# Kernel optimization log

Measured on AMD Instinct MI355X. Metric: run time of the kernel, lower is better.

The kernel has to match this reference:

```python
import jax, jax.numpy as jnp
import numpy as np


def _chamfer(xyz1, xyz2):
    # xyz1: [B, N, 3], xyz2: [B, M, 3]
    sq1 = jnp.sum(xyz1 * xyz1, axis=-1)            # [B, N]
    sq2 = jnp.sum(xyz2 * xyz2, axis=-1)            # [B, M]
    inner = jnp.einsum('bnd,bmd->bnm', xyz1, xyz2) # [B, N, M]
    d = sq1[:, :, None] + sq2[:, None, :] - 2.0 * inner
    d = jnp.maximum(d, 0.0)  # guard tiny negatives from cancellation
    dist1 = jnp.min(d, axis=2)  # [B, N] nearest in xyz2 for each point of xyz1
    dist2 = jnp.min(d, axis=1)  # [B, M]
    return jnp.mean(dist1) + jnp.mean(dist2)


def setup_inputs() -> dict:
    key = jax.random.key(0)
    k1, k2 = jax.random.split(key)
    B, N, M = 16, 4096, 4096
    xyz1 = jax.random.normal(k1, (B, N, 3), dtype=jnp.float32)
    xyz2 = jax.random.normal(k2, (B, M, 3), dtype=jnp.float32)
    return {"xyz1": xyz1, "xyz2": xyz2}


def reference(xyz1, xyz2):
    return _chamfer(xyz1, xyz2)
```

## Files before the change

kernel.cpp:

```cpp
#include <hip/hip_runtime.h>


#define BATCH 16
#define NPTS  4096
#define NQ_TOTAL (BATCH * NPTS)

typedef __attribute__((ext_vector_type(8)))  short bf16x8;
typedef __attribute__((ext_vector_type(16))) float f32x16;
typedef __attribute__((ext_vector_type(4)))  unsigned int u32x4;

union FragCast { bf16x8 v; u32x4 u; };

__device__ __forceinline__ unsigned short bf16_rne(float v) {
    unsigned u = __float_as_uint(v);
    u += 0x7FFFu + ((u >> 16) & 1u);
    return (unsigned short)(u >> 16);
}
__device__ __forceinline__ float bf16f(unsigned short h) {
    return __uint_as_float(((unsigned)h) << 16);
}

__global__ __launch_bounds__(256, 2) void chamfer_fused_kernel(
    const float* __restrict__ xyz1, const float* __restrict__ xyz2,
    float* __restrict__ partials)
{
    const int orig = (int)blockIdx.x;
    const int wfid = (orig & 7) * 64 + (orig >> 3);
    const int og = wfid & 15;
    const int b  = (wfid >> 4) & 15;
    const int d  = wfid >> 8;

    const int tid = (int)threadIdx.x;
    const int wid = tid >> 6;
    const int l   = tid & 63;
    const int c   = l & 31;
    const int g   = l >> 5;
    const int strip0 = og * 8 + wid;
    const int strip1 = og * 8 + wid + 4;

    const float* qpts = d ? xyz2 : xyz1;
    const float* tpts = d ? xyz1 : xyz2;

    const unsigned short one = 0x3F80;
    bf16x8 af0, af1;
    #pragma unroll
    for (int s = 0; s < 2; ++s) {
        const int strip = s ? strip1 : strip0;
        const int qi = b * NPTS + strip * 32 + c;
        const float qx = qpts[qi * 3 + 0];
        const float qy = qpts[qi * 3 + 1];
        const float qz = qpts[qi * 3 + 2];
        const float mx = -2.0f * qx, my = -2.0f * qy, mz = -2.0f * qz;
        const float Q  = fmaf(qx, qx, fmaf(qy, qy, qz * qz));
        const unsigned short xh = bf16_rne(mx), xl = bf16_rne(mx - bf16f(xh));
        const unsigned short yh = bf16_rne(my), yl = bf16_rne(my - bf16f(yh));
        const unsigned short zh = bf16_rne(mz), zl = bf16_rne(mz - bf16f(zh));
        const unsigned short Qh = bf16_rne(Q),  Ql = bf16_rne(Q - bf16f(Qh));
        bf16x8 af;
        if (g == 0) {
            af[0] = (short)xh; af[1] = (short)xh; af[2] = (short)xl; af[3] = (short)yh;
            af[4] = (short)yh; af[5] = (short)yl; af[6] = (short)zh; af[7] = (short)zh;
        } else {
            af[0] = (short)zl; af[1] = (short)one; af[2] = (short)one; af[3] = (short)Qh;
            af[4] = (short)Ql; af[5] = 0;          af[6] = 0;          af[7] = 0;
        }
        if (s) af1 = af; else af0 = af;
    }

    f32x16 vzero;
    #pragma unroll
    for (int i = 0; i < 16; ++i) vzero[i] = 0.0f;

    f32x16 rm0, rm1;
    #pragma unroll
    for (int i = 0; i < 16; ++i) { rm0[i] = 1e30f; rm1[i] = 1e30f; }

    __shared__ u32x4 lds[64 * 64];

    for (int cc = 0; cc < 2; ++cc) {
        __syncthreads();

        const float* tb = tpts + ((size_t)b * NPTS + (size_t)cc * 2048) * 3;
        #pragma unroll
        for (int k = 0; k < 8; ++k) {
            const int pi = k * 256 + tid;
            const float x = tb[pi * 3 + 0];
            const float y = tb[pi * 3 + 1];
            const float z = tb[pi * 3 + 2];
            const float S = fmaf(x, x, fmaf(y, y, z * z));
            const unsigned short Xh = bf16_rne(x), Xl = bf16_rne(x - bf16f(Xh));
            const unsigned short Yh = bf16_rne(y), Yl = bf16_rne(y - bf16f(Yh));
            const unsigned short Zh = bf16_rne(z), Zl = bf16_rne(z - bf16f(Zh));
            const unsigned short Sh = bf16_rne(S), Sl = bf16_rne(S - bf16f(Sh));
            FragCast f0, f1;
            f0.v[0] = (short)Xh; f0.v[1] = (short)Xl; f0.v[2] = (short)Xh; f0.v[3] = (short)Yh;
            f0.v[4] = (short)Yl; f0.v[5] = (short)Yh; f0.v[6] = (short)Zh; f0.v[7] = (short)Zl;
            f1.v[0] = (short)Zh; f1.v[1] = (short)Sh; f1.v[2] = (short)Sl; f1.v[3] = (short)one;
            f1.v[4] = (short)one; f1.v[5] = 0;        f1.v[6] = 0;         f1.v[7] = 0;
            const int t  = pi >> 5;
            const int c2 = pi & 31;
            lds[t * 64 + c2]      = f0.u;
            lds[t * 64 + 32 + c2] = f1.u;
        }
        __syncthreads();

        #pragma unroll 2
        for (int t = 0; t < 64; t += 2) {
            FragCast ta, tb2;
            ta.u  = lds[(t + 0) * 64 + l];
            tb2.u = lds[(t + 1) * 64 + l];
            f32x16 a0 = __builtin_amdgcn_mfma_f32_32x32x16_bf16(af0, ta.v,  vzero, 0, 0, 0);
            f32x16 a1 = __builtin_amdgcn_mfma_f32_32x32x16_bf16(af0, tb2.v, vzero, 0, 0, 0);
            f32x16 b0 = __builtin_amdgcn_mfma_f32_32x32x16_bf16(af1, ta.v,  vzero, 0, 0, 0);
            f32x16 b1 = __builtin_amdgcn_mfma_f32_32x32x16_bf16(af1, tb2.v, vzero, 0, 0, 0);
            #pragma unroll
            for (int i = 0; i < 16; ++i) {
                rm0[i] = fminf(fminf(rm0[i], a0[i]), a1[i]);
                rm1[i] = fminf(fminf(rm1[i], b0[i]), b1[i]);
            }
        }
    }

    #pragma unroll
    for (int m = 1; m <= 16; m <<= 1) {
        #pragma unroll
        for (int i = 0; i < 16; ++i) {
            rm0[i] = fminf(rm0[i], __shfl_xor(rm0[i], m, 64));
            rm1[i] = fminf(rm1[i], __shfl_xor(rm1[i], m, 64));
        }
    }

    float s0 = 0.0f, s1 = 0.0f;
    #pragma unroll
    for (int i = 0; i < 16; ++i) {
        s0 += fmaxf(rm0[i], 0.0f);
        s1 += fmaxf(rm1[i], 0.0f);
    }
    s0 += __shfl_xor(s0, 32, 64);
    s1 += __shfl_xor(s1, 32, 64);
    const float s = s0 + s1;

    __shared__ float wsum[4];
    if (l == 0) wsum[wid] = s;
    __syncthreads();
    if (tid == 0)
        partials[orig] = wsum[0] + wsum[1] + wsum[2] + wsum[3];
}

__global__ __launch_bounds__(256) void final_kernel(
    const float* __restrict__ partials, float* __restrict__ out)
{
    const int t = (int)threadIdx.x;
    float v = partials[t] + partials[t + 256];

    #pragma unroll
    for (int off = 32; off >= 1; off >>= 1)
        v += __shfl_down(v, off, 64);

    __shared__ float wsum[4];
    const int lane = t & 63;
    const int wid  = t >> 6;
    if (lane == 0) wsum[wid] = v;
    __syncthreads();
    if (t == 0)
        out[0] = (wsum[0] + wsum[1] + wsum[2] + wsum[3]) * (1.0f / (float)NQ_TOTAL);
}

extern "C" void kernel_launch(void* const* d_in, const int* in_sizes, int n_in,
                              void* d_out, int out_size, void* d_ws, size_t ws_size,
                              hipStream_t stream) {
    const float* xyz1 = (const float*)d_in[0];
    const float* xyz2 = (const float*)d_in[1];
    float* out = (float*)d_out;
    float* partials = (float*)d_ws;

    chamfer_fused_kernel<<<512, 256, 0, stream>>>(xyz1, xyz2, partials);
    final_kernel<<<1, 256, 0, stream>>>(partials, out);
}
```

Measured before the change: 27.08 us.

## Give each wave four query strips over half the targets, merge mins in LDS

```diff
diff --git a/kernel.cpp b/kernel.cpp
--- a/kernel.cpp
+++ b/kernel.cpp
@@ -18,6 +18,30 @@
 }
 __device__ __forceinline__ float bf16f(unsigned short h) {
     return __uint_as_float(((unsigned)h) << 16);
+}
+
+__device__ __forceinline__ bf16x8 build_af(const float* __restrict__ qpts,
+                                           int b, int strip, int c, int g) {
+    const int qi = b * NPTS + strip * 32 + c;
+    const float qx = qpts[qi * 3 + 0];
+    const float qy = qpts[qi * 3 + 1];
+    const float qz = qpts[qi * 3 + 2];
+    const float mx = -2.0f * qx, my = -2.0f * qy, mz = -2.0f * qz;
+    const float Q  = fmaf(qx, qx, fmaf(qy, qy, qz * qz));
+    const unsigned short xh = bf16_rne(mx), xl = bf16_rne(mx - bf16f(xh));
+    const unsigned short yh = bf16_rne(my), yl = bf16_rne(my - bf16f(yh));
+    const unsigned short zh = bf16_rne(mz), zl = bf16_rne(mz - bf16f(zh));
+    const unsigned short Qh = bf16_rne(Q),  Ql = bf16_rne(Q - bf16f(Qh));
+    const unsigned short one = 0x3F80;
+    bf16x8 af;
+    if (g == 0) {
+        af[0] = (short)xh; af[1] = (short)xh; af[2] = (short)xl; af[3] = (short)yh;
+        af[4] = (short)yh; af[5] = (short)yl; af[6] = (short)zh; af[7] = (short)zh;
+    } else {
+        af[0] = (short)zl; af[1] = (short)one; af[2] = (short)one; af[3] = (short)Qh;
+        af[4] = (short)Ql; af[5] = 0;          af[6] = 0;          af[7] = 0;
+    }
+    return af;
 }
 
 __global__ __launch_bounds__(256, 2) void chamfer_fused_kernel(
@@ -26,7 +50,7 @@
 {
     const int orig = (int)blockIdx.x;
     const int wfid = (orig & 7) * 64 + (orig >> 3);
-    const int og = wfid & 15;
+    const int sg = wfid & 15;
     const int b  = (wfid >> 4) & 15;
     const int d  = wfid >> 8;
 
@@ -35,58 +59,43 @@
     const int l   = tid & 63;
     const int c   = l & 31;
     const int g   = l >> 5;
-    const int strip0 = og * 8 + wid;
-    const int strip1 = og * 8 + wid + 4;
+    const int qw  = wid & 1;
+    const int h   = wid >> 1;
 
     const float* qpts = d ? xyz2 : xyz1;
     const float* tpts = d ? xyz1 : xyz2;
 
+    const bf16x8 af0 = build_af(qpts, b, sg * 8 + qw * 4 + 0, c, g);
+    const bf16x8 af1 = build_af(qpts, b, sg * 8 + qw * 4 + 1, c, g);
+    const bf16x8 af2 = build_af(qpts, b, sg * 8 + qw * 4 + 2, c, g);
+    const bf16x8 af3 = build_af(qpts, b, sg * 8 + qw * 4 + 3, c, g);
+
+    f32x16 vzero;
+    #pragma unroll
+    for (int i = 0; i < 16; ++i) vzero[i] = 0.0f;
+
+    f32x16 rm0, rm1, rm2, rm3;
+    #pragma unroll
+    for (int i = 0; i < 16; ++i) { rm0[i] = 1e30f; rm1[i] = 1e30f; rm2[i] = 1e30f; rm3[i] = 1e30f; }
+
+    __shared__ u32x4 lds[2048];
+    __shared__ float lmin[4][128];
+
     const unsigned short one = 0x3F80;
-    bf16x8 af0, af1;
-    #pragma unroll
-    for (int s = 0; s < 2; ++s) {
-        const int strip = s ? strip1 : strip0;
-        const int qi = b * NPTS + strip * 32 + c;
-        const float qx = qpts[qi * 3 + 0];
-        const float qy = qpts[qi * 3 + 1];
-        const float qz = qpts[qi * 3 + 2];
-        const float mx = -2.0f * qx, my = -2.0f * qy, mz = -2.0f * qz;
-        const float Q  = fmaf(qx, qx, fmaf(qy, qy, qz * qz));
-        const unsigned short xh = bf16_rne(mx), xl = bf16_rne(mx - bf16f(xh));
-        const unsigned short yh = bf16_rne(my), yl = bf16_rne(my - bf16f(yh));
-        const unsigned short zh = bf16_rne(mz), zl = bf16_rne(mz - bf16f(zh));
-        const unsigned short Qh = bf16_rne(Q),  Ql = bf16_rne(Q - bf16f(Qh));
-        bf16x8 af;
-        if (g == 0) {
-            af[0] = (short)xh; af[1] = (short)xh; af[2] = (short)xl; af[3] = (short)yh;
-            af[4] = (short)yh; af[5] = (short)yl; af[6] = (short)zh; af[7] = (short)zh;
-        } else {
-            af[0] = (short)zl; af[1] = (short)one; af[2] = (short)one; af[3] = (short)Qh;
-            af[4] = (short)Ql; af[5] = 0;          af[6] = 0;          af[7] = 0;
-        }
-        if (s) af1 = af; else af0 = af;
-    }
-
-    f32x16 vzero;
-    #pragma unroll
-    for (int i = 0; i < 16; ++i) vzero[i] = 0.0f;
-
-    f32x16 rm0, rm1;
-    #pragma unroll
-    for (int i = 0; i < 16; ++i) { rm0[i] = 1e30f; rm1[i] = 1e30f; }
-
-    __shared__ u32x4 lds[64 * 64];
-
-    for (int cc = 0; cc < 2; ++cc) {
+    const float* tptr = tpts + (size_t)b * NPTS * 3;
+
+    for (int p = 0; p < 4; ++p) {
         __syncthreads();
 
-        const float* tb = tpts + ((size_t)b * NPTS + (size_t)cc * 2048) * 3;
         #pragma unroll
-        for (int k = 0; k < 8; ++k) {
-            const int pi = k * 256 + tid;
-            const float x = tb[pi * 3 + 0];
-            const float y = tb[pi * 3 + 1];
-            const float z = tb[pi * 3 + 2];
+        for (int k = 0; k < 4; ++k) {
+            const int pi  = k * 256 + tid;
+            const int h2  = pi >> 9;
+            const int idx = pi & 511;
+            const int gp  = h2 * 2048 + p * 512 + idx;
+            const float x = tptr[gp * 3 + 0];
+            const float y = tptr[gp * 3 + 1];
+            const float z = tptr[gp * 3 + 2];
             const float S = fmaf(x, x, fmaf(y, y, z * z));
             const unsigned short Xh = bf16_rne(x), Xl = bf16_rne(x - bf16f(Xh));
             const unsigned short Yh = bf16_rne(y), Yl = bf16_rne(y - bf16f(Yh));
@@ -97,26 +106,36 @@
             f0.v[4] = (short)Yl; f0.v[5] = (short)Yh; f0.v[6] = (short)Zh; f0.v[7] = (short)Zl;
             f1.v[0] = (short)Zh; f1.v[1] = (short)Sh; f1.v[2] = (short)Sl; f1.v[3] = (short)one;
             f1.v[4] = (short)one; f1.v[5] = 0;        f1.v[6] = 0;         f1.v[7] = 0;
-            const int t  = pi >> 5;
-            const int c2 = pi & 31;
-            lds[t * 64 + c2]      = f0.u;
-            lds[t * 64 + 32 + c2] = f1.u;
+            const int t  = idx >> 5;
+            const int c2 = idx & 31;
+            lds[h2 * 1024 + t * 64 + c2]      = f0.u;
+            lds[h2 * 1024 + t * 64 + 32 + c2] = f1.u;
         }
         __syncthreads();
 
+        const int lbase = h * 1024 + l;
         #pragma unroll 2
-        for (int t = 0; t < 64; t += 2) {
-            FragCast ta, tb2;
-            ta.u  = lds[(t + 0) * 64 + l];
-            tb2.u = lds[(t + 1) * 64 + l];
-            f32x16 a0 = __builtin_amdgcn_mfma_f32_32x32x16_bf16(af0, ta.v,  vzero, 0, 0, 0);
-            f32x16 a1 = __builtin_amdgcn_mfma_f32_32x32x16_bf16(af0, tb2.v, vzero, 0, 0, 0);
-            f32x16 b0 = __builtin_amdgcn_mfma_f32_32x32x16_bf16(af1, ta.v,  vzero, 0, 0, 0);
-            f32x16 b1 = __builtin_amdgcn_mfma_f32_32x32x16_bf16(af1, tb2.v, vzero, 0, 0, 0);
+        for (int t = 0; t < 16; t += 2) {
+            FragCast ta, tb;
+            ta.u = lds[lbase + (t + 0) * 64];
+            tb.u = lds[lbase + (t + 1) * 64];
+            f32x16 o0a = __builtin_amdgcn_mfma_f32_32x32x16_bf16(af0, ta.v, vzero, 0, 0, 0);
+            f32x16 o0b = __builtin_amdgcn_mfma_f32_32x32x16_bf16(af0, tb.v, vzero, 0, 0, 0);
+            f32x16 o1a = __builtin_amdgcn_mfma_f32_32x32x16_bf16(af1, ta.v, vzero, 0, 0, 0);
+            f32x16 o1b = __builtin_amdgcn_mfma_f32_32x32x16_bf16(af1, tb.v, vzero, 0, 0, 0);
             #pragma unroll
             for (int i = 0; i < 16; ++i) {
-                rm0[i] = fminf(fminf(rm0[i], a0[i]), a1[i]);
-                rm1[i] = fminf(fminf(rm1[i], b0[i]), b1[i]);
+                rm0[i] = fminf(rm0[i], fminf(o0a[i], o0b[i]));
+                rm1[i] = fminf(rm1[i], fminf(o1a[i], o1b[i]));
+            }
+            f32x16 o2a = __builtin_amdgcn_mfma_f32_32x32x16_bf16(af2, ta.v, vzero, 0, 0, 0);
+            f32x16 o2b = __builtin_amdgcn_mfma_f32_32x32x16_bf16(af2, tb.v, vzero, 0, 0, 0);
+            f32x16 o3a = __builtin_amdgcn_mfma_f32_32x32x16_bf16(af3, ta.v, vzero, 0, 0, 0);
+            f32x16 o3b = __builtin_amdgcn_mfma_f32_32x32x16_bf16(af3, tb.v, vzero, 0, 0, 0);
+            #pragma unroll
+            for (int i = 0; i < 16; ++i) {
+                rm2[i] = fminf(rm2[i], fminf(o2a[i], o2b[i]));
+                rm3[i] = fminf(rm3[i], fminf(o3a[i], o3b[i]));
             }
         }
     }
@@ -127,21 +146,33 @@
         for (int i = 0; i < 16; ++i) {
             rm0[i] = fminf(rm0[i], __shfl_xor(rm0[i], m, 64));
             rm1[i] = fminf(rm1[i], __shfl_xor(rm1[i], m, 64));
-        }
-    }
-
-    float s0 = 0.0f, s1 = 0.0f;
-    #pragma unroll
-    for (int i = 0; i < 16; ++i) {
-        s0 += fmaxf(rm0[i], 0.0f);
-        s1 += fmaxf(rm1[i], 0.0f);
-    }
-    s0 += __shfl_xor(s0, 32, 64);
-    s1 += __shfl_xor(s1, 32, 64);
-    const float s = s0 + s1;
+            rm2[i] = fminf(rm2[i], __shfl_xor(rm2[i], m, 64));
+            rm3[i] = fminf(rm3[i], __shfl_xor(rm3[i], m, 64));
+        }
+    }
+
+    if (c == 0) {
+        #pragma unroll
+        for (int i = 0; i < 16; ++i) {
+            const int row = (i & 3) + 8 * (i >> 2) + 4 * g;
+            lmin[wid][0 * 32 + row] = rm0[i];
+            lmin[wid][1 * 32 + row] = rm1[i];
+            lmin[wid][2 * 32 + row] = rm2[i];
+            lmin[wid][3 * 32 + row] = rm3[i];
+        }
+    }
+    __syncthreads();
+
+    const int qw2  = tid >> 7;
+    const int idx2 = tid & 127;
+    float v = fmaxf(fminf(lmin[qw2][idx2], lmin[qw2 + 2][idx2]), 0.0f);
+
+    #pragma unroll
+    for (int off = 32; off >= 1; off >>= 1)
+        v += __shfl_down(v, off, 64);
 
     __shared__ float wsum[4];
-    if (l == 0) wsum[wid] = s;
+    if (l == 0) wsum[wid] = v;
     __syncthreads();
     if (tid == 0)
         partials[orig] = wsum[0] + wsum[1] + wsum[2] + wsum[3];
```

After: 49.01 us. 81.0% more time.

## Double-buffer target tiles in LDS, prefetching next chunk during MFMA loop

Applied to the files above, without the earlier changes.

```diff
diff --git a/kernel.cpp b/kernel.cpp
--- a/kernel.cpp
+++ b/kernel.cpp
@@ -18,6 +18,23 @@
 }
 __device__ __forceinline__ float bf16f(unsigned short h) {
     return __uint_as_float(((unsigned)h) << 16);
+}
+
+__device__ __forceinline__ void pack_pt(float x, float y, float z,
+                                        u32x4* f0u, u32x4* f1u) {
+    const float S = fmaf(x, x, fmaf(y, y, z * z));
+    const unsigned short Xh = bf16_rne(x), Xl = bf16_rne(x - bf16f(Xh));
+    const unsigned short Yh = bf16_rne(y), Yl = bf16_rne(y - bf16f(Yh));
+    const unsigned short Zh = bf16_rne(z), Zl = bf16_rne(z - bf16f(Zh));
+    const unsigned short Sh = bf16_rne(S), Sl = bf16_rne(S - bf16f(Sh));
+    const unsigned short one = 0x3F80;
+    FragCast f0, f1;
+    f0.v[0] = (short)Xh; f0.v[1] = (short)Xl; f0.v[2] = (short)Xh; f0.v[3] = (short)Yh;
+    f0.v[4] = (short)Yl; f0.v[5] = (short)Yh; f0.v[6] = (short)Zh; f0.v[7] = (short)Zl;
+    f1.v[0] = (short)Zh; f1.v[1] = (short)Sh; f1.v[2] = (short)Sl; f1.v[3] = (short)one;
+    f1.v[4] = (short)one; f1.v[5] = 0;        f1.v[6] = 0;         f1.v[7] = 0;
+    *f0u = f0.u;
+    *f1u = f1.u;
 }
 
 __global__ __launch_bounds__(256, 2) void chamfer_fused_kernel(
@@ -33,7 +50,7 @@
     const int tid = (int)threadIdx.x;
     const int wid = tid >> 6;
     const int l   = tid & 63;
-    const int c   = l & 31;
+    const int lc  = l & 31;
     const int g   = l >> 5;
     const int strip0 = og * 8 + wid;
     const int strip1 = og * 8 + wid + 4;
@@ -46,7 +63,7 @@
     #pragma unroll
     for (int s = 0; s < 2; ++s) {
         const int strip = s ? strip1 : strip0;
-        const int qi = b * NPTS + strip * 32 + c;
+        const int qi = b * NPTS + strip * 32 + lc;
         const float qx = qpts[qi * 3 + 0];
         const float qy = qpts[qi * 3 + 1];
         const float qz = qpts[qi * 3 + 2];
@@ -75,50 +92,69 @@
     #pragma unroll
     for (int i = 0; i < 16; ++i) { rm0[i] = 1e30f; rm1[i] = 1e30f; }
 
-    __shared__ u32x4 lds[64 * 64];
-
-    for (int cc = 0; cc < 2; ++cc) {
-        __syncthreads();
-
-        const float* tb = tpts + ((size_t)b * NPTS + (size_t)cc * 2048) * 3;
-        #pragma unroll
-        for (int k = 0; k < 8; ++k) {
-            const int pi = k * 256 + tid;
-            const float x = tb[pi * 3 + 0];
-            const float y = tb[pi * 3 + 1];
-            const float z = tb[pi * 3 + 2];
-            const float S = fmaf(x, x, fmaf(y, y, z * z));
-            const unsigned short Xh = bf16_rne(x), Xl = bf16_rne(x - bf16f(Xh));
-            const unsigned short Yh = bf16_rne(y), Yl = bf16_rne(y - bf16f(Yh));
-            const unsigned short Zh = bf16_rne(z), Zl = bf16_rne(z - bf16f(Zh));
-            const unsigned short Sh = bf16_rne(S), Sl = bf16_rne(S - bf16f(Sh));
-            FragCast f0, f1;
-            f0.v[0] = (short)Xh; f0.v[1] = (short)Xl; f0.v[2] = (short)Xh; f0.v[3] = (short)Yh;
-            f0.v[4] = (short)Yl; f0.v[5] = (short)Yh; f0.v[6] = (short)Zh; f0.v[7] = (short)Zl;
-            f1.v[0] = (short)Zh; f1.v[1] = (short)Sh; f1.v[2] = (short)Sl; f1.v[3] = (short)one;
-            f1.v[4] = (short)one; f1.v[5] = 0;        f1.v[6] = 0;         f1.v[7] = 0;
-            const int t  = pi >> 5;
-            const int c2 = pi & 31;
-            lds[t * 64 + c2]      = f0.u;
-            lds[t * 64 + 32 + c2] = f1.u;
-        }
-        __syncthreads();
+    __shared__ u32x4 lds[2][32 * 64];
+
+    const float* tptr = tpts + (size_t)b * NPTS * 3;
+
+    #pragma unroll
+    for (int k = 0; k < 4; ++k) {
+        const int pi = k * 256 + tid;
+        const float x = tptr[pi * 3 + 0];
+        const float y = tptr[pi * 3 + 1];
+        const float z = tptr[pi * 3 + 2];
+        u32x4 f0u, f1u;
+        pack_pt(x, y, z, &f0u, &f1u);
+        const int t  = pi >> 5;
+        const int c2 = pi & 31;
+        lds[0][t * 64 + c2]      = f0u;
+        lds[0][t * 64 + 32 + c2] = f1u;
+    }
+    __syncthreads();
+
+    #pragma unroll
+    for (int cc = 0; cc < 4; ++cc) {
+        const int cur = cc & 1;
+
+        float px[4], py[4], pz[4];
+        if (cc < 3) {
+            #pragma unroll
+            for (int k = 0; k < 4; ++k) {
+                const int gp = (cc + 1) * 1024 + k * 256 + tid;
+                px[k] = tptr[gp * 3 + 0];
+                py[k] = tptr[gp * 3 + 1];
+                pz[k] = tptr[gp * 3 + 2];
+            }
+        }
 
         #pragma unroll 2
-        for (int t = 0; t < 64; t += 2) {
+        for (int t = 0; t < 32; t += 2) {
             FragCast ta, tb2;
-            ta.u  = lds[(t + 0) * 64 + l];
-            tb2.u = lds[(t + 1) * 64 + l];
+            ta.u  = lds[cur][(t + 0) * 64 + l];
+            tb2.u = lds[cur][(t + 1) * 64 + l];
             f32x16 a0 = __builtin_amdgcn_mfma_f32_32x32x16_bf16(af0, ta.v,  vzero, 0, 0, 0);
             f32x16 a1 = __builtin_amdgcn_mfma_f32_32x32x16_bf16(af0, tb2.v, vzero, 0, 0, 0);
             f32x16 b0 = __builtin_amdgcn_mfma_f32_32x32x16_bf16(af1, ta.v,  vzero, 0, 0, 0);
             f32x16 b1 = __builtin_amdgcn_mfma_f32_32x32x16_bf16(af1, tb2.v, vzero, 0, 0, 0);
             #pragma unroll
             for (int i = 0; i < 16; ++i) {
-                rm0[i] = fminf(fminf(rm0[i], a0[i]), a1[i]);
-                rm1[i] = fminf(fminf(rm1[i], b0[i]), b1[i]);
+                rm0[i] = fminf(rm0[i], fminf(a0[i], a1[i]));
+                rm1[i] = fminf(rm1[i], fminf(b0[i], b1[i]));
             }
         }
+
+        if (cc < 3) {
+            #pragma unroll
+            for (int k = 0; k < 4; ++k) {
+                const int pi = k * 256 + tid;
+                u32x4 f0u, f1u;
+                pack_pt(px[k], py[k], pz[k], &f0u, &f1u);
+                const int t  = pi >> 5;
+                const int c2 = pi & 31;
+                lds[cur ^ 1][t * 64 + c2]      = f0u;
+                lds[cur ^ 1][t * 64 + 32 + c2] = f1u;
+            }
+        }
+        __syncthreads();
     }
 
     #pragma unroll
```

Result: slower. 42.56 us (+57.2%).

## Split target loop across two wave halves with 512-thread blocks and LDS min merge

Applied to the files above, without the earlier changes.

```diff
diff --git a/kernel.cpp b/kernel.cpp
--- a/kernel.cpp
+++ b/kernel.cpp
@@ -20,7 +20,7 @@
     return __uint_as_float(((unsigned)h) << 16);
 }
 
-__global__ __launch_bounds__(256, 2) void chamfer_fused_kernel(
+__global__ __launch_bounds__(512, 4) void chamfer_fused_kernel(
     const float* __restrict__ xyz1, const float* __restrict__ xyz2,
     float* __restrict__ partials)
 {
@@ -33,10 +33,12 @@
     const int tid = (int)threadIdx.x;
     const int wid = tid >> 6;
     const int l   = tid & 63;
-    const int c   = l & 31;
+    const int lc  = l & 31;
     const int g   = l >> 5;
-    const int strip0 = og * 8 + wid;
-    const int strip1 = og * 8 + wid + 4;
+    const int wq  = wid & 3;
+    const int h   = wid >> 2;
+    const int strip0 = og * 8 + wq;
+    const int strip1 = og * 8 + wq + 4;
 
     const float* qpts = d ? xyz2 : xyz1;
     const float* tpts = d ? xyz1 : xyz2;
@@ -46,7 +48,7 @@
     #pragma unroll
     for (int s = 0; s < 2; ++s) {
         const int strip = s ? strip1 : strip0;
-        const int qi = b * NPTS + strip * 32 + c;
+        const int qi = b * NPTS + strip * 32 + lc;
         const float qx = qpts[qi * 3 + 0];
         const float qy = qpts[qi * 3 + 1];
         const float qz = qpts[qi * 3 + 2];
@@ -76,14 +78,17 @@
     for (int i = 0; i < 16; ++i) { rm0[i] = 1e30f; rm1[i] = 1e30f; }
 
     __shared__ u32x4 lds[64 * 64];
+    __shared__ float lmin[8][64];
+
+    const float* tptr = tpts + (size_t)b * NPTS * 3;
 
     for (int cc = 0; cc < 2; ++cc) {
         __syncthreads();
 
-        const float* tb = tpts + ((size_t)b * NPTS + (size_t)cc * 2048) * 3;
-        #pragma unroll
-        for (int k = 0; k < 8; ++k) {
-            const int pi = k * 256 + tid;
+        const float* tb = tptr + (size_t)cc * 2048 * 3;
+        #pragma unroll
+        for (int k = 0; k < 4; ++k) {
+            const int pi = k * 512 + tid;
             const float x = tb[pi * 3 + 0];
             const float y = tb[pi * 3 + 1];
             const float z = tb[pi * 3 + 2];
@@ -104,8 +109,9 @@
         }
         __syncthreads();
 
+        const int t0 = h * 32;
         #pragma unroll 2
-        for (int t = 0; t < 64; t += 2) {
+        for (int t = t0; t < t0 + 32; t += 2) {
             FragCast ta, tb2;
             ta.u  = lds[(t + 0) * 64 + l];
             tb2.u = lds[(t + 1) * 64 + l];
@@ -115,8 +121,8 @@
             f32x16 b1 = __builtin_amdgcn_mfma_f32_32x32x16_bf16(af1, tb2.v, vzero, 0, 0, 0);
             #pragma unroll
             for (int i = 0; i < 16; ++i) {
-                rm0[i] = fminf(fminf(rm0[i], a0[i]), a1[i]);
-                rm1[i] = fminf(fminf(rm1[i], b0[i]), b1[i]);
+                rm0[i] = fminf(rm0[i], fminf(a0[i], a1[i]));
+                rm1[i] = fminf(rm1[i], fminf(b0[i], b1[i]));
             }
         }
     }
@@ -130,21 +136,38 @@
         }
     }
 
-    float s0 = 0.0f, s1 = 0.0f;
-    #pragma unroll
-    for (int i = 0; i < 16; ++i) {
-        s0 += fmaxf(rm0[i], 0.0f);
-        s1 += fmaxf(rm1[i], 0.0f);
-    }
-    s0 += __shfl_xor(s0, 32, 64);
-    s1 += __shfl_xor(s1, 32, 64);
-    const float s = s0 + s1;
-
-    __shared__ float wsum[4];
-    if (l == 0) wsum[wid] = s;
+    if (lc == 0) {
+        #pragma unroll
+        for (int i = 0; i < 16; ++i) {
+            const int row = (i & 3) + 8 * (i >> 2) + 4 * g;
+            lmin[wid][0 * 32 + row] = rm0[i];
+            lmin[wid][1 * 32 + row] = rm1[i];
+        }
+    }
     __syncthreads();
-    if (tid == 0)
-        partials[orig] = wsum[0] + wsum[1] + wsum[2] + wsum[3];
+
+    float v = 0.0f;
+    if (tid < 256) {
+        const int s = tid >> 5;
+        const int r = tid & 31;
+        const int quad = s & 3;
+        const int slot = s >> 2;
+        v = fmaxf(fminf(lmin[quad][slot * 32 + r], lmin[quad + 4][slot * 32 + r]), 0.0f);
+    }
+
+    #pragma unroll
+    for (int off = 32; off >= 1; off >>= 1)
+        v += __shfl_down(v, off, 64);
+
+    __shared__ float wsum[8];
+    if (l == 0) wsum[wid] = v;
+    __syncthreads();
+    if (tid == 0) {
+        float s = 0.0f;
+        #pragma unroll
+        for (int w = 0; w < 8; ++w) s += wsum[w];
+        partials[orig] = s;
+    }
 }
 
 __global__ __launch_bounds__(256) void final_kernel(
@@ -174,6 +197,6 @@
     float* out = (float*)d_out;
     float* partials = (float*)d_ws;
 
-    chamfer_fused_kernel<<<512, 256, 0, stream>>>(xyz1, xyz2, partials);
+    chamfer_fused_kernel<<<512, 512, 0, stream>>>(xyz1, xyz2, partials);
     final_kernel<<<1, 256, 0, stream>>>(partials, out);
 }
```

Measured after the change: 54.57 us. +101.5%, slower.
